# Kernel optimization log

Hardware: AMD Instinct MI355X
Metric: run time of the kernel (lower is better)

## Reference

```python
import jax, jax.numpy as jnp
import numpy as np

B = 8192
I = 1024
H = 1024


def _xavier(key, out_dim, in_dim):
    limit = float(np.sqrt(6.0 / (in_dim + out_dim)))
    return jax.random.uniform(key, (out_dim, in_dim), jnp.float32, -limit, limit)


def setup_inputs() -> dict:
    key = jax.random.key(0)
    ks = jax.random.split(key, 16)
    inp = {
        "x": jax.random.normal(ks[0], (B, I), jnp.float32),
        "h_prev": jax.random.normal(ks[1], (B, H), jnp.float32),
        "c_prev": jax.random.normal(ks[2], (B, H), jnp.float32),
        # input->hidden weights (hidden_size, input_size), hidden->hidden (hidden_size, hidden_size)
        "Wxi": _xavier(ks[3], H, I), "Whi": _xavier(ks[4], H, H),
        "Wxf": _xavier(ks[5], H, I), "Whf": _xavier(ks[6], H, H),
        "Wxc": _xavier(ks[7], H, I), "Whc": _xavier(ks[8], H, H),
        "Wxo": _xavier(ks[9], H, I), "Who": _xavier(ks[10], H, H),
        "bxi": jnp.zeros((H,), jnp.float32), "bhi": jnp.zeros((H,), jnp.float32),
        # forget-gate biases initialized to ones per _init_weights
        "bxf": jnp.ones((H,), jnp.float32), "bhf": jnp.ones((H,), jnp.float32),
        "bxc": jnp.zeros((H,), jnp.float32), "bhc": jnp.zeros((H,), jnp.float32),
        "bxo": jnp.zeros((H,), jnp.float32), "bho": jnp.zeros((H,), jnp.float32),
    }
    return inp


def reference(x, h_prev, c_prev,
              Wxi, Whi, Wxf, Whf, Wxc, Whc, Wxo, Who,
              bxi, bhi, bxf, bhf, bxc, bhc, bxo, bho):
    # Fuse the 8 small linears into two GEMMs: stack along the output (gate) axis.
    Wx = jnp.concatenate([Wxi, Wxf, Wxc, Wxo], axis=0)   # (4H, I)
    Wh = jnp.concatenate([Whi, Whf, Whc, Who], axis=0)   # (4H, H)
    bx = jnp.concatenate([bxi, bxf, bxc, bxo], axis=0)    # (4H,)
    bh = jnp.concatenate([bhi, bhf, bhc, bho], axis=0)    # (4H,)
    gates = x @ Wx.T + h_prev @ Wh.T + (bx + bh)           # (B, 4H)
    zi, zf, zc, zo = jnp.split(gates, 4, axis=1)
    i = jax.nn.sigmoid(zi)
    f = jax.nn.sigmoid(zf)
    g = jnp.tanh(zc)
    o = jax.nn.sigmoid(zo)
    c_new = f * c_prev + i * g
    h_new = o * jnp.tanh(c_new)
    return (h_new, c_new)
```

## Files before the change

### kernel.cpp

```cpp
#include <hip/hip_runtime.h>
#include <hip/hip_bf16.h>
#include <stdint.h>


#define B_DIM 8192
#define I_DIM 1024
#define H_DIM 1024
#define K_DIM 2048
#define N_DIM 4096

typedef short bf16x8 __attribute__((ext_vector_type(8)));
typedef float f32x4 __attribute__((ext_vector_type(4)));

__device__ __forceinline__ unsigned short f2bf(float f) {
  unsigned int u = __float_as_uint(f);
  u += 0x7FFFu + ((u >> 16) & 1u);
  return (unsigned short)(u >> 16);
}

__global__ void pack_A_kernel(const float* __restrict__ x,
                              const float* __restrict__ h,
                              unsigned short* __restrict__ outA) {
  const int total = B_DIM * K_DIM / 8;
  for (int idx = blockIdx.x * blockDim.x + threadIdx.x; idx < total;
       idx += gridDim.x * blockDim.x) {
    int row = idx >> 8;
    int col = (idx & 255) * 8;
    const float* src = (col < I_DIM) ? (x + (size_t)row * I_DIM + col)
                                     : (h + (size_t)row * H_DIM + (col - I_DIM));
    const float4* s4 = (const float4*)src;
    float4 v0 = s4[0], v1 = s4[1];
    bf16x8 o;
    o[0] = f2bf(v0.x); o[1] = f2bf(v0.y); o[2] = f2bf(v0.z); o[3] = f2bf(v0.w);
    o[4] = f2bf(v1.x); o[5] = f2bf(v1.y); o[6] = f2bf(v1.z); o[7] = f2bf(v1.w);
    *(bf16x8*)(outA + (size_t)idx * 8) = o;
  }
}

__global__ void pack_B_kernel(const float* __restrict__ Wxi, const float* __restrict__ Whi,
                              const float* __restrict__ Wxf, const float* __restrict__ Whf,
                              const float* __restrict__ Wxc, const float* __restrict__ Whc,
                              const float* __restrict__ Wxo, const float* __restrict__ Who,
                              unsigned short* __restrict__ outB) {
  const int total = N_DIM * K_DIM / 8;
  for (int idx = blockIdx.x * blockDim.x + threadIdx.x; idx < total;
       idx += gridDim.x * blockDim.x) {
    int r = idx >> 8;
    int k = (idx & 255) * 8;
    int g = (r >> 4) & 3;
    int h = ((r >> 6) << 4) | (r & 15);
    const float* base;
    if (k < I_DIM) {
      base = (g == 0) ? Wxi : (g == 1) ? Wxf : (g == 2) ? Wxc : Wxo;
      base += (size_t)h * I_DIM + k;
    } else {
      base = (g == 0) ? Whi : (g == 1) ? Whf : (g == 2) ? Whc : Who;
      base += (size_t)h * H_DIM + (k - I_DIM);
    }
    const float4* s4 = (const float4*)base;
    float4 v0 = s4[0], v1 = s4[1];
    bf16x8 o;
    o[0] = f2bf(v0.x); o[1] = f2bf(v0.y); o[2] = f2bf(v0.z); o[3] = f2bf(v0.w);
    o[4] = f2bf(v1.x); o[5] = f2bf(v1.y); o[6] = f2bf(v1.z); o[7] = f2bf(v1.w);
    *(bf16x8*)(outB + (size_t)idx * 8) = o;
  }
}

__launch_bounds__(256, 2)
__global__ void lstm_gemm_kernel(const unsigned short* __restrict__ A,
                                 const unsigned short* __restrict__ Bp,
                                 const float* __restrict__ c_prev,
                                 const float* __restrict__ bxi, const float* __restrict__ bhi,
                                 const float* __restrict__ bxf, const float* __restrict__ bhf,
                                 const float* __restrict__ bxc, const float* __restrict__ bhc,
                                 const float* __restrict__ bxo, const float* __restrict__ bho,
                                 float* __restrict__ out) {
  __shared__ __align__(16) char sA[128 * 64 * 2];
  __shared__ __align__(16) char sB[128 * 64 * 2];

  const int nwg = gridDim.x;
  int bid = blockIdx.x;
  int q = nwg >> 3;
  int wg = (bid & 7) * q + (bid >> 3);
  int bm = wg >> 5;
  int bn = wg & 31;

  int tid = threadIdx.x;
  int lane = tid & 63;
  int wid = tid >> 6;
  int wm = wid >> 1;
  int wn = wid & 1;

  int srow = lane >> 3;
  int scol = (lane & 7) ^ srow;
  const unsigned short* gA = A + (size_t)(bm * 128 + wid * 8 + srow) * K_DIM + scol * 8;
  const unsigned short* gB = Bp + (size_t)(bn * 128 + wid * 8 + srow) * K_DIM + scol * 8;
  char* lA = sA + wid * 1024;
  char* lB = sB + wid * 1024;

  f32x4 acc[4][4];
  f32x4 zero = {0.f, 0.f, 0.f, 0.f};
#pragma unroll
  for (int m = 0; m < 4; ++m)
#pragma unroll
    for (int n = 0; n < 4; ++n) acc[m][n] = zero;

  int c15 = lane & 15;
  int kl = lane >> 4;
  int swz = (lane & 7) << 4;
  int rAb = wm * 64 + c15;
  int rBb = wn * 64 + c15;

  for (int kt = 0; kt < K_DIM / 64; ++kt) {
#pragma unroll
    for (int i = 0; i < 4; ++i) {
      __builtin_amdgcn_global_load_lds(
          (const __attribute__((address_space(1))) void*)(gA + (size_t)i * 32 * K_DIM + kt * 64),
          (__attribute__((address_space(3))) void*)(lA + i * 4096), 16, 0, 0);
      __builtin_amdgcn_global_load_lds(
          (const __attribute__((address_space(1))) void*)(gB + (size_t)i * 32 * K_DIM + kt * 64),
          (__attribute__((address_space(3))) void*)(lB + i * 4096), 16, 0, 0);
    }
    asm volatile("s_waitcnt vmcnt(0)" ::: "memory");
    __syncthreads();

#pragma unroll
    for (int kk = 0; kk < 2; ++kk) {
      bf16x8 af[4], bfr[4];
#pragma unroll
      for (int m = 0; m < 4; ++m)
        af[m] = *(const bf16x8*)(sA + (rAb + m * 16) * 128 + ((((kk << 2) | kl) << 4) ^ swz));
#pragma unroll
      for (int n = 0; n < 4; ++n)
        bfr[n] = *(const bf16x8*)(sB + (rBb + n * 16) * 128 + ((((kk << 2) | kl) << 4) ^ swz));
#pragma unroll
      for (int m = 0; m < 4; ++m)
#pragma unroll
        for (int n = 0; n < 4; ++n)
          acc[m][n] = __builtin_amdgcn_mfma_f32_16x16x32_bf16(af[m], bfr[n], acc[m][n], 0, 0, 0);
    }
    __syncthreads();
  }

  int h = (bn * 2 + wn) * 16 + c15;
  float bi = bxi[h] + bhi[h];
  float bf_ = bxf[h] + bhf[h];
  float bc = bxc[h] + bhc[h];
  float bo = bxo[h] + bho[h];
  int row0 = bm * 128 + wm * 64 + kl * 4;
#pragma unroll
  for (int m = 0; m < 4; ++m) {
#pragma unroll
    for (int j = 0; j < 4; ++j) {
      int r = row0 + m * 16 + j;
      size_t off = (size_t)r * H_DIM + h;
      float zi = acc[m][0][j] + bi;
      float zf = acc[m][1][j] + bf_;
      float zc = acc[m][2][j] + bc;
      float zo = acc[m][3][j] + bo;
      float ig = 1.f / (1.f + __expf(-zi));
      float fg = 1.f / (1.f + __expf(-zf));
      float e2 = __expf(-2.f * zc);
      float gg = (1.f - e2) / (1.f + e2);
      float og = 1.f / (1.f + __expf(-zo));
      float cp = c_prev[off];
      float cn = fg * cp + ig * gg;
      float e2c = __expf(-2.f * cn);
      float th = (1.f - e2c) / (1.f + e2c);
      out[off] = og * th;
      out[(size_t)B_DIM * H_DIM + off] = cn;
    }
  }
}

extern "C" void kernel_launch(void* const* d_in, const int* in_sizes, int n_in,
                              void* d_out, int out_size, void* d_ws, size_t ws_size,
                              hipStream_t stream) {
  const float* x      = (const float*)d_in[0];
  const float* h_prev = (const float*)d_in[1];
  const float* c_prev = (const float*)d_in[2];
  const float* Wxi = (const float*)d_in[3];
  const float* Whi = (const float*)d_in[4];
  const float* Wxf = (const float*)d_in[5];
  const float* Whf = (const float*)d_in[6];
  const float* Wxc = (const float*)d_in[7];
  const float* Whc = (const float*)d_in[8];
  const float* Wxo = (const float*)d_in[9];
  const float* Who = (const float*)d_in[10];
  const float* bxi = (const float*)d_in[11];
  const float* bhi = (const float*)d_in[12];
  const float* bxf = (const float*)d_in[13];
  const float* bhf = (const float*)d_in[14];
  const float* bxc = (const float*)d_in[15];
  const float* bhc = (const float*)d_in[16];
  const float* bxo = (const float*)d_in[17];
  const float* bho = (const float*)d_in[18];

  unsigned short* Abf = (unsigned short*)d_ws;
  unsigned short* Bbf = (unsigned short*)((char*)d_ws + (size_t)B_DIM * K_DIM * 2);

  pack_A_kernel<<<2048, 256, 0, stream>>>(x, h_prev, Abf);
  pack_B_kernel<<<1024, 256, 0, stream>>>(Wxi, Whi, Wxf, Whf, Wxc, Whc, Wxo, Who, Bbf);
  lstm_gemm_kernel<<<2048, 256, 0, stream>>>(Abf, Bbf, c_prev,
      bxi, bhi, bxf, bhf, bxc, bhc, bxo, bho, (float*)d_out);
}
```

Before: 180.8 us.

## Use 256x256 tiles with 8 waves and double-buffered async LDS pipeline

Replaces the 128x128 tile GEMM, which loads synchronously and waits with vmcnt(0) every step, with a 256x256 tile per 512-thread block. The new version uses double-buffered global_load_lds prefetch two k-tiles ahead and splits each k-tile into four MFMA quadrants interleaved with LDS reads and staging. It also raises wave priority with s_setprio around the MFMA bursts. The aim is to hide global-load latency, improve operand reuse, and cut barrier stalls. The cost is 128KB of LDS per block and a 128-float accumulator array per thread, which limits occupancy and raises register pressure.

```diff
diff --git a/kernel.cpp b/kernel.cpp
--- a/kernel.cpp
+++ b/kernel.cpp
@@ -8,6 +8,7 @@
 #define H_DIM 1024
 #define K_DIM 2048
 #define N_DIM 4096
+#define NKT   32
 
 typedef short bf16x8 __attribute__((ext_vector_type(8)));
 typedef float f32x4 __attribute__((ext_vector_type(4)));
@@ -66,7 +67,76 @@
   }
 }
 
-__launch_bounds__(256, 2)
+
+#define STAGE(gptr, slotoff, ktile) do {                                          \
+    int _ktc = (ktile) < NKT ? (ktile) : (NKT - 1);                               \
+    const unsigned short* _g = (gptr) + (size_t)_ktc * 64;                        \
+    __builtin_amdgcn_global_load_lds(                                             \
+        (const __attribute__((address_space(1))) void*)_g,                        \
+        (__attribute__((address_space(3))) void*)(lds + (slotoff) + wid * 1024),  \
+        16, 0, 0);                                                                \
+    __builtin_amdgcn_global_load_lds(                                             \
+        (const __attribute__((address_space(1))) void*)(_g + (size_t)64 * K_DIM), \
+        (__attribute__((address_space(3))) void*)(lds + (slotoff) + 8192 + wid * 1024), \
+        16, 0, 0);                                                                \
+  } while (0)
+
+#define MFMAQ(MH, GH, BARR)                                                       \
+  _Pragma("unroll") for (int m = 0; m < 4; ++m)                                   \
+  _Pragma("unroll") for (int nn = 0; nn < 2; ++nn)                                \
+  _Pragma("unroll") for (int kk = 0; kk < 2; ++kk)                                \
+    acc[(MH)*4 + m][(GH)*2 + nn] = __builtin_amdgcn_mfma_f32_16x16x32_bf16(       \
+        Af[m][kk], BARR[nn][kk], acc[(MH)*4 + m][(GH)*2 + nn], 0, 0, 0)
+
+#define KTILE(BUF, KT) do {                                                       \
+    const int _bo = (BUF) * 32768;                                                \
+                       \
+    _Pragma("unroll") for (int m = 0; m < 4; ++m) {                               \
+      Af[m][0] = *(const bf16x8*)(ldsAr + _bo + m * 2048 + rd0);                  \
+      Af[m][1] = *(const bf16x8*)(ldsAr + _bo + m * 2048 + rd1); }                \
+    _Pragma("unroll") for (int nn = 0; nn < 2; ++nn) {                            \
+      Bl[nn][0] = *(const bf16x8*)(ldsBr + _bo + nn * 2048 + rd0);                \
+      Bl[nn][1] = *(const bf16x8*)(ldsBr + _bo + nn * 2048 + rd1); }              \
+    __builtin_amdgcn_s_barrier();                                                 \
+    asm volatile("s_waitcnt lgkmcnt(0)");                                         \
+    __builtin_amdgcn_s_setprio(1);                                                \
+    MFMAQ(0, 0, Bl);                                                              \
+    __builtin_amdgcn_s_setprio(0);                                                \
+    __builtin_amdgcn_s_barrier();                                                 \
+                                                              \
+    _Pragma("unroll") for (int nn = 0; nn < 2; ++nn) {                            \
+      Bh[nn][0] = *(const bf16x8*)(ldsBr + _bo + 4096 + nn * 2048 + rd0);         \
+      Bh[nn][1] = *(const bf16x8*)(ldsBr + _bo + 4096 + nn * 2048 + rd1); }       \
+    __builtin_amdgcn_s_barrier();                                                 \
+    asm volatile("s_waitcnt lgkmcnt(0)");                                         \
+    __builtin_amdgcn_s_setprio(1);                                                \
+    MFMAQ(0, 1, Bh);                                                              \
+    __builtin_amdgcn_s_setprio(0);                                                \
+    __builtin_amdgcn_s_barrier();                                                 \
+               \
+    _Pragma("unroll") for (int m = 0; m < 4; ++m) {                               \
+      Af[m][0] = *(const bf16x8*)(ldsAr + _bo + 8192 + m * 2048 + rd0);           \
+      Af[m][1] = *(const bf16x8*)(ldsAr + _bo + 8192 + m * 2048 + rd1); }         \
+    STAGE(gB0p, 65536 + _bo, (KT) + 2);                                           \
+    STAGE(gB1p, 65536 + _bo + 16384, (KT) + 2);                                   \
+    __builtin_amdgcn_s_barrier();                                                 \
+    asm volatile("s_waitcnt lgkmcnt(0)");                                         \
+    __builtin_amdgcn_s_setprio(1);                                                \
+    MFMAQ(1, 1, Bh);                                                              \
+    __builtin_amdgcn_s_setprio(0);                                                \
+    __builtin_amdgcn_s_barrier();                                                 \
+                       \
+    STAGE(gA0p, _bo, (KT) + 2);                                                   \
+    STAGE(gA1p, _bo + 16384, (KT) + 2);                                           \
+    __builtin_amdgcn_s_barrier();                                                 \
+    __builtin_amdgcn_s_setprio(1);                                                \
+    MFMAQ(1, 0, Bl);                                                              \
+    __builtin_amdgcn_s_setprio(0);                                                \
+    asm volatile("s_waitcnt vmcnt(8)" ::: "memory");                              \
+    __builtin_amdgcn_s_barrier();                                                 \
+  } while (0)
+
+__launch_bounds__(512, 2)
 __global__ void lstm_gemm_kernel(const unsigned short* __restrict__ A,
                                  const unsigned short* __restrict__ Bp,
                                  const float* __restrict__ c_prev,
@@ -75,89 +145,79 @@
                                  const float* __restrict__ bxc, const float* __restrict__ bhc,
                                  const float* __restrict__ bxo, const float* __restrict__ bho,
                                  float* __restrict__ out) {
-  __shared__ __align__(16) char sA[128 * 64 * 2];
-  __shared__ __align__(16) char sB[128 * 64 * 2];
+  __shared__ __align__(16) char lds[131072];
 
   const int nwg = gridDim.x;
   int bid = blockIdx.x;
   int q = nwg >> 3;
   int wg = (bid & 7) * q + (bid >> 3);
-  int bm = wg >> 5;
-  int bn = wg & 31;
+  int bm = wg >> 4;
+  int bn = wg & 15;
 
   int tid = threadIdx.x;
   int lane = tid & 63;
   int wid = tid >> 6;
-  int wm = wid >> 1;
-  int wn = wid & 1;
+  int wm = wid >> 2;
+  int wn = wid & 3;
 
   int srow = lane >> 3;
-  int scol = (lane & 7) ^ srow;
-  const unsigned short* gA = A + (size_t)(bm * 128 + wid * 8 + srow) * K_DIM + scol * 8;
-  const unsigned short* gB = Bp + (size_t)(bn * 128 + wid * 8 + srow) * K_DIM + scol * 8;
-  char* lA = sA + wid * 1024;
-  char* lB = sB + wid * 1024;
-
-  f32x4 acc[4][4];
-  f32x4 zero = {0.f, 0.f, 0.f, 0.f};
-#pragma unroll
-  for (int m = 0; m < 4; ++m)
-#pragma unroll
-    for (int n = 0; n < 4; ++n) acc[m][n] = zero;
+  int schunk = (lane & 7) ^ srow;
+  const unsigned short* gA0p = A  + (size_t)(bm * 256 + wid * 8 + srow) * K_DIM + schunk * 8;
+  const unsigned short* gA1p = gA0p + (size_t)128 * K_DIM;
+  const unsigned short* gB0p = Bp + (size_t)(bn * 256 + wid * 8 + srow) * K_DIM + schunk * 8;
+  const unsigned short* gB1p = gB0p + (size_t)128 * K_DIM;
 
   int c15 = lane & 15;
   int kl = lane >> 4;
-  int swz = (lane & 7) << 4;
-  int rAb = wm * 64 + c15;
-  int rBb = wn * 64 + c15;
-
-  for (int kt = 0; kt < K_DIM / 64; ++kt) {
-#pragma unroll
-    for (int i = 0; i < 4; ++i) {
-      __builtin_amdgcn_global_load_lds(
-          (const __attribute__((address_space(1))) void*)(gA + (size_t)i * 32 * K_DIM + kt * 64),
-          (__attribute__((address_space(3))) void*)(lA + i * 4096), 16, 0, 0);
-      __builtin_amdgcn_global_load_lds(
-          (const __attribute__((address_space(1))) void*)(gB + (size_t)i * 32 * K_DIM + kt * 64),
-          (__attribute__((address_space(3))) void*)(lB + i * 4096), 16, 0, 0);
-    }
-    asm volatile("s_waitcnt vmcnt(0)" ::: "memory");
-    __syncthreads();
-
-#pragma unroll
-    for (int kk = 0; kk < 2; ++kk) {
-      bf16x8 af[4], bfr[4];
-#pragma unroll
-      for (int m = 0; m < 4; ++m)
-        af[m] = *(const bf16x8*)(sA + (rAb + m * 16) * 128 + ((((kk << 2) | kl) << 4) ^ swz));
-#pragma unroll
-      for (int n = 0; n < 4; ++n)
-        bfr[n] = *(const bf16x8*)(sB + (rBb + n * 16) * 128 + ((((kk << 2) | kl) << 4) ^ swz));
-#pragma unroll
-      for (int m = 0; m < 4; ++m)
-#pragma unroll
-        for (int n = 0; n < 4; ++n)
-          acc[m][n] = __builtin_amdgcn_mfma_f32_16x16x32_bf16(af[m], bfr[n], acc[m][n], 0, 0, 0);
-    }
-    __syncthreads();
-  }
-
-  int h = (bn * 2 + wn) * 16 + c15;
+  const char* ldsAr = lds + wm * 16384 + c15 * 128;
+  const char* ldsBr = lds + 65536 + (wn >> 1) * 16384 + ((wn & 1) * 64 + c15) * 128;
+  int rd0 = ((kl) ^ (lane & 7)) << 4;
+  int rd1 = ((4 | kl) ^ (lane & 7)) << 4;
+
+  f32x4 acc[8][4];
+  f32x4 zero = {0.f, 0.f, 0.f, 0.f};
+#pragma unroll
+  for (int m = 0; m < 8; ++m)
+#pragma unroll
+    for (int n = 0; n < 4; ++n) acc[m][n] = zero;
+
+  bf16x8 Af[4][2];
+  bf16x8 Bl[2][2];
+  bf16x8 Bh[2][2];
+
+  STAGE(gA0p, 0, 0);
+  STAGE(gA1p, 16384, 0);
+  STAGE(gB0p, 65536, 0);
+  STAGE(gB1p, 65536 + 16384, 0);
+  STAGE(gA0p, 32768, 1);
+  STAGE(gA1p, 32768 + 16384, 1);
+  STAGE(gB0p, 65536 + 32768, 1);
+  STAGE(gB1p, 65536 + 32768 + 16384, 1);
+  asm volatile("s_waitcnt vmcnt(8)" ::: "memory");
+  __builtin_amdgcn_s_barrier();
+
+#pragma unroll 1
+  for (int kt = 0; kt < NKT; kt += 2) {
+    KTILE(0, kt);
+    KTILE(1, kt + 1);
+  }
+
+  int h = (bn * 4 + wn) * 16 + c15;
   float bi = bxi[h] + bhi[h];
   float bf_ = bxf[h] + bhf[h];
   float bc = bxc[h] + bhc[h];
   float bo = bxo[h] + bho[h];
-  int row0 = bm * 128 + wm * 64 + kl * 4;
-#pragma unroll
-  for (int m = 0; m < 4; ++m) {
+  int row0 = bm * 256 + wm * 128 + kl * 4;
+#pragma unroll
+  for (int mi = 0; mi < 8; ++mi) {
 #pragma unroll
     for (int j = 0; j < 4; ++j) {
-      int r = row0 + m * 16 + j;
+      int r = row0 + mi * 16 + j;
       size_t off = (size_t)r * H_DIM + h;
-      float zi = acc[m][0][j] + bi;
-      float zf = acc[m][1][j] + bf_;
-      float zc = acc[m][2][j] + bc;
-      float zo = acc[m][3][j] + bo;
+      float zi = acc[mi][0][j] + bi;
+      float zf = acc[mi][1][j] + bf_;
+      float zc = acc[mi][2][j] + bc;
+      float zo = acc[mi][3][j] + bo;
       float ig = 1.f / (1.f + __expf(-zi));
       float fg = 1.f / (1.f + __expf(-zf));
       float e2 = __expf(-2.f * zc);
@@ -201,6 +261,6 @@
 
   pack_A_kernel<<<2048, 256, 0, stream>>>(x, h_prev, Abf);
   pack_B_kernel<<<1024, 256, 0, stream>>>(Wxi, Whi, Wxf, Whf, Wxc, Whc, Wxo, Who, Bbf);
-  lstm_gemm_kernel<<<2048, 256, 0, stream>>>(Abf, Bbf, c_prev,
+  lstm_gemm_kernel<<<512, 512, 0, stream>>>(Abf, Bbf, c_prev,
       bxi, bhi, bxf, bhf, bxc, bhc, bxo, bho, (float*)d_out);
 }
```

New measurement: 167.0 us. -7.6%, faster.

## Use 256x256 tiles with register-resident B fragments and double-buffered LDS A

Applied to the files above, without the earlier changes.

The GEMM now uses 256x256 output tiles with 8 waves per workgroup. The B weights are pre-packed into MFMA fragment order so each wave loads its B operands straight from global memory into registers, prefetching one k-tile ahead. Only A is staged through double-buffered, swizzled LDS using register-staged loads, which leaves one barrier per k-tile, and s_setprio is raised around the MFMA bursts. The two pack kernels are merged into one launch. This cuts LDS traffic and barrier overhead and raises operand reuse, at the cost of many more accumulator registers (128 floats per lane) and uncoalesced per-wave B fetches from global/L2.

```diff
diff --git a/kernel.cpp b/kernel.cpp
--- a/kernel.cpp
+++ b/kernel.cpp
@@ -8,6 +8,7 @@
 #define H_DIM 1024
 #define K_DIM 2048
 #define N_DIM 4096
+#define NKT   32
 
 typedef short bf16x8 __attribute__((ext_vector_type(8)));
 typedef float f32x4 __attribute__((ext_vector_type(4)));
@@ -18,55 +19,85 @@
   return (unsigned short)(u >> 16);
 }
 
-__global__ void pack_A_kernel(const float* __restrict__ x,
-                              const float* __restrict__ h,
-                              unsigned short* __restrict__ outA) {
-  const int total = B_DIM * K_DIM / 8;
+__global__ void pack_AB_kernel(const float* __restrict__ x, const float* __restrict__ h,
+                               const float* __restrict__ Wxi, const float* __restrict__ Whi,
+                               const float* __restrict__ Wxf, const float* __restrict__ Whf,
+                               const float* __restrict__ Wxc, const float* __restrict__ Whc,
+                               const float* __restrict__ Wxo, const float* __restrict__ Who,
+                               unsigned short* __restrict__ outA,
+                               unsigned short* __restrict__ outB) {
+  const int totalA = B_DIM * K_DIM / 8;
+  const int total  = totalA + N_DIM * K_DIM / 8;
   for (int idx = blockIdx.x * blockDim.x + threadIdx.x; idx < total;
        idx += gridDim.x * blockDim.x) {
-    int row = idx >> 8;
-    int col = (idx & 255) * 8;
-    const float* src = (col < I_DIM) ? (x + (size_t)row * I_DIM + col)
-                                     : (h + (size_t)row * H_DIM + (col - I_DIM));
+    const float* src;
+    unsigned short* dst;
+    if (idx < totalA) {
+      int row = idx >> 8;
+      int col = (idx & 255) * 8;
+      src = (col < I_DIM) ? (x + (size_t)row * I_DIM + col)
+                          : (h + (size_t)row * H_DIM + (col - I_DIM));
+      dst = outA + (size_t)idx * 8;
+    } else {
+      int u2 = idx - totalA;
+      int lane_ = u2 & 63, nn = (u2 >> 6) & 3, kk = (u2 >> 8) & 1;
+      int kt = (u2 >> 9) & 31, wn = (u2 >> 14) & 3, bn = u2 >> 16;
+      int r = bn * 256 + wn * 64 + nn * 16 + (lane_ & 15);
+      int k = kt * 64 + kk * 32 + (lane_ >> 4) * 8;
+      int g = (r >> 4) & 3;
+      int hh = ((r >> 6) << 4) | (r & 15);
+      src = (k < I_DIM)
+          ? ((g == 0 ? Wxi : g == 1 ? Wxf : g == 2 ? Wxc : Wxo) + (size_t)hh * I_DIM + k)
+          : ((g == 0 ? Whi : g == 1 ? Whf : g == 2 ? Whc : Who) + (size_t)hh * H_DIM + (k - I_DIM));
+      dst = outB + (size_t)u2 * 8;
+    }
     const float4* s4 = (const float4*)src;
     float4 v0 = s4[0], v1 = s4[1];
     bf16x8 o;
     o[0] = f2bf(v0.x); o[1] = f2bf(v0.y); o[2] = f2bf(v0.z); o[3] = f2bf(v0.w);
     o[4] = f2bf(v1.x); o[5] = f2bf(v1.y); o[6] = f2bf(v1.z); o[7] = f2bf(v1.w);
-    *(bf16x8*)(outA + (size_t)idx * 8) = o;
-  }
-}
-
-__global__ void pack_B_kernel(const float* __restrict__ Wxi, const float* __restrict__ Whi,
-                              const float* __restrict__ Wxf, const float* __restrict__ Whf,
-                              const float* __restrict__ Wxc, const float* __restrict__ Whc,
-                              const float* __restrict__ Wxo, const float* __restrict__ Who,
-                              unsigned short* __restrict__ outB) {
-  const int total = N_DIM * K_DIM / 8;
-  for (int idx = blockIdx.x * blockDim.x + threadIdx.x; idx < total;
-       idx += gridDim.x * blockDim.x) {
-    int r = idx >> 8;
-    int k = (idx & 255) * 8;
-    int g = (r >> 4) & 3;
-    int h = ((r >> 6) << 4) | (r & 15);
-    const float* base;
-    if (k < I_DIM) {
-      base = (g == 0) ? Wxi : (g == 1) ? Wxf : (g == 2) ? Wxc : Wxo;
-      base += (size_t)h * I_DIM + k;
-    } else {
-      base = (g == 0) ? Whi : (g == 1) ? Whf : (g == 2) ? Whc : Who;
-      base += (size_t)h * H_DIM + (k - I_DIM);
-    }
-    const float4* s4 = (const float4*)base;
-    float4 v0 = s4[0], v1 = s4[1];
-    bf16x8 o;
-    o[0] = f2bf(v0.x); o[1] = f2bf(v0.y); o[2] = f2bf(v0.z); o[3] = f2bf(v0.w);
-    o[4] = f2bf(v1.x); o[5] = f2bf(v1.y); o[6] = f2bf(v1.z); o[7] = f2bf(v1.w);
-    *(bf16x8*)(outB + (size_t)idx * 8) = o;
-  }
-}
-
-__launch_bounds__(256, 2)
+    *(bf16x8*)dst = o;
+  }
+}
+
+
+#define QUAD(MH, KOFF, BR) do {                                               \
+    bf16x8 aq[4];                                                             \
+    _Pragma("unroll") for (int mf = 0; mf < 4; ++mf)                          \
+      aq[mf] = *(const bf16x8*)(ldsAr + _bo + (MH)*8192 + mf * 2048 + (KOFF));\
+    __builtin_amdgcn_s_setprio(1);                                            \
+    _Pragma("unroll") for (int mf = 0; mf < 4; ++mf)                          \
+    _Pragma("unroll") for (int nn = 0; nn < 4; ++nn)                          \
+      acc[(MH)*4 + mf][nn] = __builtin_amdgcn_mfma_f32_16x16x32_bf16(         \
+          aq[mf], BR[nn], acc[(MH)*4 + mf][nn], 0, 0, 0);                     \
+    __builtin_amdgcn_s_setprio(0);                                            \
+  } while (0)
+
+#define KTILE(BUF, KT, BC0, BN0) do {                                         \
+    const int _bo  = (BUF) * 32768;                                           \
+    const int _bo1 = ((BUF) ^ 1) * 32768;                                     \
+    int _kt1 = (KT) + 1 < NKT ? (KT) + 1 : NKT - 1;                           \
+    const unsigned short* _ga = gAst + (size_t)_kt1 * 64;                     \
+    bf16x8 ar0 = *(const bf16x8*)(_ga);                                       \
+    bf16x8 ar1 = *(const bf16x8*)(_ga + 8);                                   \
+    bf16x8 ar2 = *(const bf16x8*)(_ga + 16);                                  \
+    bf16x8 ar3 = *(const bf16x8*)(_ga + 24);                                  \
+    _Pragma("unroll") for (int nn = 0; nn < 4; ++nn)                          \
+      Bk1[nn] = *(const bf16x8*)(gBfr + (size_t)(KT) * 4096 + 2048 + nn*512); \
+    _Pragma("unroll") for (int nn = 0; nn < 4; ++nn)                          \
+      BN0[nn] = *(const bf16x8*)(gBfr + (size_t)_kt1 * 4096 + nn * 512);      \
+    QUAD(0, rd0, BC0);                                                        \
+    QUAD(1, rd0, BC0);                                                        \
+    *(bf16x8*)(ldsAw + _bo1 + woff0) = ar0;                                   \
+    *(bf16x8*)(ldsAw + _bo1 + woff1) = ar1;                                   \
+    QUAD(0, rd1, Bk1);                                                        \
+    QUAD(1, rd1, Bk1);                                                        \
+    *(bf16x8*)(ldsAw + _bo1 + woff2) = ar2;                                   \
+    *(bf16x8*)(ldsAw + _bo1 + woff3) = ar3;                                   \
+    __syncthreads();                                                          \
+  } while (0)
+
+__launch_bounds__(512, 2)
 __global__ void lstm_gemm_kernel(const unsigned short* __restrict__ A,
                                  const unsigned short* __restrict__ Bp,
                                  const float* __restrict__ c_prev,
@@ -75,89 +106,83 @@
                                  const float* __restrict__ bxc, const float* __restrict__ bhc,
                                  const float* __restrict__ bxo, const float* __restrict__ bho,
                                  float* __restrict__ out) {
-  __shared__ __align__(16) char sA[128 * 64 * 2];
-  __shared__ __align__(16) char sB[128 * 64 * 2];
+  __shared__ __align__(16) char lds[65536];
 
   const int nwg = gridDim.x;
   int bid = blockIdx.x;
   int q = nwg >> 3;
   int wg = (bid & 7) * q + (bid >> 3);
-  int bm = wg >> 5;
-  int bn = wg & 31;
+  int bm = wg >> 4;
+  int bn = wg & 15;
 
   int tid = threadIdx.x;
   int lane = tid & 63;
   int wid = tid >> 6;
-  int wm = wid >> 1;
-  int wn = wid & 1;
-
-  int srow = lane >> 3;
-  int scol = (lane & 7) ^ srow;
-  const unsigned short* gA = A + (size_t)(bm * 128 + wid * 8 + srow) * K_DIM + scol * 8;
-  const unsigned short* gB = Bp + (size_t)(bn * 128 + wid * 8 + srow) * K_DIM + scol * 8;
-  char* lA = sA + wid * 1024;
-  char* lB = sB + wid * 1024;
-
-  f32x4 acc[4][4];
-  f32x4 zero = {0.f, 0.f, 0.f, 0.f};
-#pragma unroll
-  for (int m = 0; m < 4; ++m)
-#pragma unroll
-    for (int n = 0; n < 4; ++n) acc[m][n] = zero;
+  int wm = wid >> 2;
+  int wn = wid & 3;
+
+  const unsigned short* gAst = A + (size_t)(bm * 256 + (tid >> 1)) * K_DIM + (tid & 1) * 32;
+  char* ldsAw = lds + (tid >> 1) * 128;
+  int wr7 = (tid >> 1) & 7;
+  int woff0 = ((((tid & 1) * 4 + 0) ^ wr7) << 4);
+  int woff1 = ((((tid & 1) * 4 + 1) ^ wr7) << 4);
+  int woff2 = ((((tid & 1) * 4 + 2) ^ wr7) << 4);
+  int woff3 = ((((tid & 1) * 4 + 3) ^ wr7) << 4);
+
+  const unsigned short* gBfr = Bp + (size_t)(bn * 4 + wn) * 131072 + lane * 8;
 
   int c15 = lane & 15;
   int kl = lane >> 4;
-  int swz = (lane & 7) << 4;
-  int rAb = wm * 64 + c15;
-  int rBb = wn * 64 + c15;
-
-  for (int kt = 0; kt < K_DIM / 64; ++kt) {
-#pragma unroll
-    for (int i = 0; i < 4; ++i) {
-      __builtin_amdgcn_global_load_lds(
-          (const __attribute__((address_space(1))) void*)(gA + (size_t)i * 32 * K_DIM + kt * 64),
-          (__attribute__((address_space(3))) void*)(lA + i * 4096), 16, 0, 0);
-      __builtin_amdgcn_global_load_lds(
-          (const __attribute__((address_space(1))) void*)(gB + (size_t)i * 32 * K_DIM + kt * 64),
-          (__attribute__((address_space(3))) void*)(lB + i * 4096), 16, 0, 0);
-    }
-    asm volatile("s_waitcnt vmcnt(0)" ::: "memory");
-    __syncthreads();
-
-#pragma unroll
-    for (int kk = 0; kk < 2; ++kk) {
-      bf16x8 af[4], bfr[4];
-#pragma unroll
-      for (int m = 0; m < 4; ++m)
-        af[m] = *(const bf16x8*)(sA + (rAb + m * 16) * 128 + ((((kk << 2) | kl) << 4) ^ swz));
-#pragma unroll
-      for (int n = 0; n < 4; ++n)
-        bfr[n] = *(const bf16x8*)(sB + (rBb + n * 16) * 128 + ((((kk << 2) | kl) << 4) ^ swz));
-#pragma unroll
-      for (int m = 0; m < 4; ++m)
-#pragma unroll
-        for (int n = 0; n < 4; ++n)
-          acc[m][n] = __builtin_amdgcn_mfma_f32_16x16x32_bf16(af[m], bfr[n], acc[m][n], 0, 0, 0);
-    }
-    __syncthreads();
-  }
-
-  int h = (bn * 2 + wn) * 16 + c15;
+  const char* ldsAr = lds + wm * 16384 + c15 * 128;
+  int rd0 = ((kl) ^ (lane & 7)) << 4;
+  int rd1 = ((4 | kl) ^ (lane & 7)) << 4;
+
+  f32x4 acc[8][4];
+  f32x4 zero = {0.f, 0.f, 0.f, 0.f};
+#pragma unroll
+  for (int m = 0; m < 8; ++m)
+#pragma unroll
+    for (int n = 0; n < 4; ++n) acc[m][n] = zero;
+
+  bf16x8 Bk0A[4], Bk0B[4], Bk1[4];
+
+#pragma unroll
+  for (int nn = 0; nn < 4; ++nn)
+    Bk0A[nn] = *(const bf16x8*)(gBfr + nn * 512);
+  {
+    bf16x8 a0 = *(const bf16x8*)(gAst);
+    bf16x8 a1 = *(const bf16x8*)(gAst + 8);
+    bf16x8 a2 = *(const bf16x8*)(gAst + 16);
+    bf16x8 a3 = *(const bf16x8*)(gAst + 24);
+    *(bf16x8*)(ldsAw + woff0) = a0;
+    *(bf16x8*)(ldsAw + woff1) = a1;
+    *(bf16x8*)(ldsAw + woff2) = a2;
+    *(bf16x8*)(ldsAw + woff3) = a3;
+  }
+  __syncthreads();
+
+#pragma unroll 1
+  for (int kt = 0; kt < NKT; kt += 2) {
+    KTILE(0, kt, Bk0A, Bk0B);
+    KTILE(1, kt + 1, Bk0B, Bk0A);
+  }
+
+  int h = (bn * 4 + wn) * 16 + c15;
   float bi = bxi[h] + bhi[h];
   float bf_ = bxf[h] + bhf[h];
   float bc = bxc[h] + bhc[h];
   float bo = bxo[h] + bho[h];
-  int row0 = bm * 128 + wm * 64 + kl * 4;
-#pragma unroll
-  for (int m = 0; m < 4; ++m) {
+  int row0 = bm * 256 + wm * 128 + kl * 4;
+#pragma unroll
+  for (int mi = 0; mi < 8; ++mi) {
 #pragma unroll
     for (int j = 0; j < 4; ++j) {
-      int r = row0 + m * 16 + j;
+      int r = row0 + mi * 16 + j;
       size_t off = (size_t)r * H_DIM + h;
-      float zi = acc[m][0][j] + bi;
-      float zf = acc[m][1][j] + bf_;
-      float zc = acc[m][2][j] + bc;
-      float zo = acc[m][3][j] + bo;
+      float zi = acc[mi][0][j] + bi;
+      float zf = acc[mi][1][j] + bf_;
+      float zc = acc[mi][2][j] + bc;
+      float zo = acc[mi][3][j] + bo;
       float ig = 1.f / (1.f + __expf(-zi));
       float fg = 1.f / (1.f + __expf(-zf));
       float e2 = __expf(-2.f * zc);
@@ -199,8 +224,8 @@
   unsigned short* Abf = (unsigned short*)d_ws;
   unsigned short* Bbf = (unsigned short*)((char*)d_ws + (size_t)B_DIM * K_DIM * 2);
 
-  pack_A_kernel<<<2048, 256, 0, stream>>>(x, h_prev, Abf);
-  pack_B_kernel<<<1024, 256, 0, stream>>>(Wxi, Whi, Wxf, Whf, Wxc, Whc, Wxo, Who, Bbf);
-  lstm_gemm_kernel<<<2048, 256, 0, stream>>>(Abf, Bbf, c_prev,
+  pack_AB_kernel<<<2048, 256, 0, stream>>>(x, h_prev,
+      Wxi, Whi, Wxf, Whf, Wxc, Whc, Wxo, Who, Abf, Bbf);
+  lstm_gemm_kernel<<<512, 512, 0, stream>>>(Abf, Bbf, c_prev,
       bxi, bhi, bxf, bhf, bxc, bhc, bxo, bho, (float*)d_out);
 }
```

Result: faster. 163.8 us (-9.4%).
